# Kernel tuning notes

Hardware: AMD Instinct MI355X
Metric: run time of the kernel (lower is better)

## Reference

```python
import jax, jax.numpy as jnp
import numpy as np
import math

DIM = 1024
N_HEADS = 16
HEAD_DIM = DIM // N_HEADS
MAX_LEN = 4096
THETA = 10000.0
LN_EPS = 1e-5


def _rope_tables(dim, max_len, theta=THETA):
    # matches precompute_rope: freqs over even indices, angles = outer(t, freqs)
    inv = 1.0 / theta ** (np.arange(0, dim, 2, dtype=np.float32) / dim)
    t = np.arange(max_len, dtype=np.float32)
    ang = np.outer(t, inv)  # [max_len, dim//2]
    return jnp.asarray(np.cos(ang)), jnp.asarray(np.sin(ang))


def setup_inputs() -> dict:
    key = jax.random.key(0)
    ks = jax.random.split(key, 5)
    B, T, D = 2, 2048, DIM
    s = 1.0 / math.sqrt(D)
    x = jax.random.normal(ks[0], (B, T, D), dtype=jnp.float32)
    wq = jax.random.normal(ks[1], (D, D), dtype=jnp.float32) * s
    wk = jax.random.normal(ks[2], (D, D), dtype=jnp.float32) * s
    wv = jax.random.normal(ks[3], (D, D), dtype=jnp.float32) * s
    wo = jax.random.normal(ks[4], (D, D), dtype=jnp.float32) * s
    ln_g = jnp.ones((D,), dtype=jnp.float32)
    ln_b = jnp.zeros((D,), dtype=jnp.float32)
    cos, sin = _rope_tables(HEAD_DIM, MAX_LEN)
    return {"x": x, "wq": wq, "wk": wk, "wv": wv, "wo": wo,
            "ln_g": ln_g, "ln_b": ln_b, "cos": cos, "sin": sin}


def _rotate(x, cos, sin):
    # x: [B, T, H, hd]; complex multiply on interleaved (even, odd) pairs
    B, T, H, hd = x.shape
    xr = x.reshape(B, T, H, hd // 2, 2)
    x0, x1 = xr[..., 0], xr[..., 1]
    c = cos[None, :T, None, :]
    s = sin[None, :T, None, :]
    o0 = x0 * c - x1 * s
    o1 = x0 * s + x1 * c
    return jnp.stack([o0, o1], axis=-1).reshape(B, T, H, hd)


def reference(x, wq, wk, wv, wo, ln_g, ln_b, cos, sin):
    B, T, D = x.shape
    H, hd = N_HEADS, HEAD_DIM
    # LayerNorm
    mu = jnp.mean(x, axis=-1, keepdims=True)
    var = jnp.var(x, axis=-1, keepdims=True)
    h = (x - mu) * jax.lax.rsqrt(var + LN_EPS) * ln_g + ln_b
    # QKV projections (torch Linear: h @ W.T)
    q = jnp.einsum('btd,ed->bte', h, wq).reshape(B, T, H, hd)
    k = jnp.einsum('btd,ed->bte', h, wk).reshape(B, T, H, hd)
    v = jnp.einsum('btd,ed->bte', h, wv).reshape(B, T, H, hd)
    q = _rotate(q, cos, sin)
    k = _rotate(k, cos, sin)
    # full (non-causal) attention, scores [B, H, T, T]
    scores = jnp.einsum('bqhd,bkhd->bhqk', q, k) / math.sqrt(hd)
    attn = jax.nn.softmax(scores, axis=-1)
    out = jnp.einsum('bhqk,bkhd->bqhd', attn, v).reshape(B, T, D)
    return jnp.einsum('btd,ed->bte', out, wo)
```

## Files before the change

### kernel.cpp

```cpp
#include <hip/hip_runtime.h>
#include <hip/hip_bf16.h>

typedef __attribute__((ext_vector_type(4))) float          fx4;
typedef __attribute__((ext_vector_type(8))) __bf16         bfx8;
typedef __attribute__((ext_vector_type(8))) unsigned short usx8;
typedef __attribute__((ext_vector_type(4))) unsigned short usx4;

#define TLEN 2048
#define ROWS 4096
#define D    1024

__device__ __forceinline__ float bf2f(unsigned short u) {
    union { unsigned int i; float f; } v; v.i = ((unsigned int)u) << 16; return v.f;
}
__device__ __forceinline__ unsigned short f2bf(float f) {
    union { float f; unsigned int i; } v; v.f = f;
    unsigned int r = v.i + 0x7fffu + ((v.i >> 16) & 1u);
    return (unsigned short)(r >> 16);
}
__device__ __forceinline__ unsigned int cvtpk_bf16(float lo, float hi) {
    unsigned int r;
    asm("v_cvt_pk_bf16_f32 %0, %1, %2" : "=v"(r) : "v"(lo), "v"(hi));
    return r;
}
__device__ __forceinline__ float fast_cos(float a) {
    float r; asm("v_cos_f32 %0, %1" : "=v"(r) : "v"(a)); return r;
}
__device__ __forceinline__ float fast_sin(float a) {
    float r; asm("v_sin_f32 %0, %1" : "=v"(r) : "v"(a)); return r;
}
__device__ __forceinline__ void gload_lds16(const unsigned short* g, unsigned short* l) {
    __builtin_amdgcn_global_load_lds((const __attribute__((address_space(1))) void*)g,
                                     (__attribute__((address_space(3))) void*)l, 16, 0, 0);
}

__device__ __forceinline__ usx4 cvt4(fx4 a) {
    usx4 o;
    #pragma unroll
    for (int j = 0; j < 4; j++) o[j] = f2bf(a[j]);
    return o;
}
__global__ __launch_bounds__(256) void prep_kernel(const float* __restrict__ x,
                                                   const float* __restrict__ g,
                                                   const float* __restrict__ bta,
                                                   const float* __restrict__ wq, const float* __restrict__ wk,
                                                   const float* __restrict__ wv, const float* __restrict__ wo,
                                                   unsigned short* __restrict__ hout,
                                                   unsigned short* __restrict__ wqkv,
                                                   unsigned short* __restrict__ wob) {
    const int tid = threadIdx.x;
    if (blockIdx.x >= 4096) {
        const int i = (blockIdx.x - 4096) * 256 + tid;
        ((usx4*)wqkv)[i]          = cvt4(((const fx4*)wq)[i]);
        ((usx4*)wqkv)[262144 + i] = cvt4(((const fx4*)wk)[i]);
        ((usx4*)wqkv)[524288 + i] = cvt4(((const fx4*)wv)[i]);
        ((usx4*)wob)[i]           = cvt4(((const fx4*)wo)[i]);
        return;
    }
    const int row = blockIdx.x;
    fx4 v = ((const fx4*)(x + (size_t)row * D))[tid];
    float s  = v[0] + v[1] + v[2] + v[3];
    float s2 = v[0]*v[0] + v[1]*v[1] + v[2]*v[2] + v[3]*v[3];
    #pragma unroll
    for (int mk = 32; mk >= 1; mk >>= 1) { s += __shfl_xor(s, mk); s2 += __shfl_xor(s2, mk); }
    __shared__ float red[8];
    const int wave = tid >> 6, lane = tid & 63;
    if (lane == 0) { red[wave] = s; red[4 + wave] = s2; }
    __syncthreads();
    s  = red[0] + red[1] + red[2] + red[3];
    s2 = red[4] + red[5] + red[6] + red[7];
    float mu   = s * (1.0f / D);
    float var  = s2 * (1.0f / D) - mu * mu;
    float rstd = rsqrtf(var + 1e-5f);
    fx4 gv = ((const fx4*)g)[tid];
    fx4 bv = ((const fx4*)bta)[tid];
    usx4 o;
    #pragma unroll
    for (int j = 0; j < 4; j++) o[j] = f2bf((v[j] - mu) * rstd * gv[j] + bv[j]);
    ((usx4*)hout)[(size_t)row * 256 + tid] = o;
}

__global__ __launch_bounds__(256) void qkvt_gemm(const unsigned short* __restrict__ hbuf,
                                                 const unsigned short* __restrict__ wqkv,
                                                 unsigned short* __restrict__ qkout,
                                                 unsigned short* __restrict__ vtout) {
    constexpr int K = 1024;
    __shared__ __align__(16) unsigned short As[128 * 32];
    __shared__ __align__(16) unsigned short Bs[128 * 32];
    const int tid = threadIdx.x, lane = tid & 63, wave = tid >> 6;
    const int fr = lane & 15, fq = lane >> 4;
    const int wr = wave >> 1, wc = wave & 1;

    const int id = blockIdx.x;
    const bool isqk = id < 512;
    int bm, bn;
    const unsigned short *Ab, *Bb;
    if (isqk) {
        bm = id & 31; bn = id >> 5;
        Ab = hbuf + (size_t)(bm * 128) * K;
        Bb = wqkv + (size_t)(bn * 128) * K;
    } else {
        int j = id - 512; bm = j & 7; bn = j >> 3;
        Ab = wqkv + (size_t)(2048 * 1024) + (size_t)(bm * 128) * K;
        Bb = hbuf + (size_t)(bn * 128) * K;
    }

    const int str0 = wave * 32 + (lane >> 2);
    const int stc  = (lane & 3) * 8;

    fx4 acc[4][4];
    #pragma unroll
    for (int m = 0; m < 4; m++)
        #pragma unroll
        for (int n = 0; n < 4; n++) acc[m][n] = (fx4)0.0f;

    for (int kt = 0; kt < K; kt += 32) {
        gload_lds16(Ab + (size_t)str0 * K + kt + stc,        &As[str0 * 32 + stc]);
        gload_lds16(Ab + (size_t)(str0 + 16) * K + kt + stc, &As[(str0 + 16) * 32 + stc]);
        gload_lds16(Bb + (size_t)str0 * K + kt + stc,        &Bs[str0 * 32 + stc]);
        gload_lds16(Bb + (size_t)(str0 + 16) * K + kt + stc, &Bs[(str0 + 16) * 32 + stc]);
        __syncthreads();
        bfx8 aF[4], bF[4];
        #pragma unroll
        for (int m = 0; m < 4; m++) aF[m] = *(const bfx8*)&As[(wr * 64 + m * 16 + fr) * 32 + fq * 8];
        #pragma unroll
        for (int n = 0; n < 4; n++) bF[n] = *(const bfx8*)&Bs[(wc * 64 + n * 16 + fr) * 32 + fq * 8];
        #pragma unroll
        for (int m = 0; m < 4; m++)
            #pragma unroll
            for (int n = 0; n < 4; n++)
                acc[m][n] = __builtin_amdgcn_mfma_f32_16x16x32_bf16(aF[m], bF[n], acc[m][n], 0, 0, 0);
        __syncthreads();
    }

    const int row0 = bm * 128 + wr * 64 + fq * 4;
    const int col0 = bn * 128 + wc * 64 + fr;
    if (isqk) {
        const float QS = 0.125f * 1.44269504088896f;
        const bool isq = bn < 8;
        const float sgn = (fr & 1) ? 1.0f : -1.0f;
        float fp[4];
        #pragma unroll
        for (int n = 0; n < 4; n++) {
            float pif = (float)(n * 8 + (fr >> 1));
            fp[n] = __builtin_amdgcn_exp2f(fmaf(pif, -0.415241011861f, -2.651496129472f));
        }
        #pragma unroll
        for (int m = 0; m < 4; m++) {
            const int rbase = row0 + m * 16;
            const float tf = (float)(rbase & (TLEN - 1));
            #pragma unroll
            for (int n = 0; n < 4; n++) {
                #pragma unroll
                for (int j = 0; j < 4; j++) {
                    float a = __builtin_amdgcn_fractf((tf + (float)j) * fp[n]);
                    float c = fast_cos(a), s = fast_sin(a);
                    float self = acc[m][n][j];
                    float other = __shfl_xor(self, 1);
                    float o = self * c + other * (sgn * s);
                    if (isq) o *= QS;
                    qkout[(size_t)(rbase + j) * 2048 + col0 + n * 16] = f2bf(o);
                }
            }
        }
    } else {
        const int bb = bn >> 4;
        #pragma unroll
        for (int m = 0; m < 4; m++)
            #pragma unroll
            for (int n = 0; n < 4; n++) {
                const int t = (col0 + n * 16) & (TLEN - 1);
                const int tp = (t & ~63) | ((n >> 1) * 32 + ((fr >> 2)) * 8 + ((n & 1)) * 4 + (fr & 3));
                #pragma unroll
                for (int j = 0; j < 4; j++) {
                    const int d = row0 + m * 16 + j;
                    vtout[(((size_t)(bb * 16 + (d >> 6)) * 64) + (d & 63)) * TLEN + tp] = f2bf(acc[m][n][j]);
                }
            }
    }
}

__global__ __launch_bounds__(256) void gemm_out64(const unsigned short* __restrict__ A,
                                                  const unsigned short* __restrict__ B,
                                                  float* __restrict__ C) {
    constexpr int K = 1024;
    __shared__ __align__(16) unsigned short As[128 * 32];
    __shared__ __align__(16) unsigned short Bs[64 * 32];
    const int tid = threadIdx.x, lane = tid & 63, wave = tid >> 6;
    const int fr = lane & 15, fq = lane >> 4;
    const int bm = blockIdx.x, bn = blockIdx.y;
    const int wr = wave >> 1, wc = wave & 1;

    const int strA = wave * 32 + (lane >> 2);
    const int strB = wave * 16 + (lane >> 2);
    const int stc  = (lane & 3) * 8;
    const unsigned short* Ab = A + (size_t)(bm * 128) * K;
    const unsigned short* Bb = B + (size_t)(bn * 64) * K;

    fx4 acc[4][2];
    #pragma unroll
    for (int m = 0; m < 4; m++)
        #pragma unroll
        for (int n = 0; n < 2; n++) acc[m][n] = (fx4)0.0f;

    for (int kt = 0; kt < K; kt += 32) {
        gload_lds16(Ab + (size_t)strA * K + kt + stc,        &As[strA * 32 + stc]);
        gload_lds16(Ab + (size_t)(strA + 16) * K + kt + stc, &As[(strA + 16) * 32 + stc]);
        gload_lds16(Bb + (size_t)strB * K + kt + stc,        &Bs[strB * 32 + stc]);
        __syncthreads();
        bfx8 aF[4], bF[2];
        #pragma unroll
        for (int m = 0; m < 4; m++) aF[m] = *(const bfx8*)&As[(wr * 64 + m * 16 + fr) * 32 + fq * 8];
        #pragma unroll
        for (int n = 0; n < 2; n++) bF[n] = *(const bfx8*)&Bs[(wc * 32 + n * 16 + fr) * 32 + fq * 8];
        #pragma unroll
        for (int m = 0; m < 4; m++)
            #pragma unroll
            for (int n = 0; n < 2; n++)
                acc[m][n] = __builtin_amdgcn_mfma_f32_16x16x32_bf16(aF[m], bF[n], acc[m][n], 0, 0, 0);
        __syncthreads();
    }

    const int row0 = bm * 128 + wr * 64 + fq * 4;
    const int col0 = bn * 64 + wc * 32 + fr;
    #pragma unroll
    for (int m = 0; m < 4; m++)
        #pragma unroll
        for (int n = 0; n < 2; n++)
            #pragma unroll
            for (int j = 0; j < 4; j++)
                C[(size_t)(row0 + m * 16 + j) * 1024 + col0 + n * 16] = acc[m][n][j];
}

__global__ __launch_bounds__(256) void attn_kernel(const unsigned short* __restrict__ qk,
                                                   const unsigned short* __restrict__ vt,
                                                   unsigned short* __restrict__ ao) {
    const int flat = blockIdx.x + (blockIdx.y << 4);
    const int sid  = (flat & 7) * 64 + (flat >> 3);
    const int qt = sid & 15, bh = sid >> 4;
    const int b = bh >> 4, hh = bh & 15;
    const int tid = threadIdx.x, lane = tid & 63, wave = tid >> 6;
    const int fr = lane & 15, fq = lane >> 4;

    __shared__ __align__(16) unsigned short sK[2][64 * 64];
    __shared__ __align__(16) unsigned short sVt[2][64 * 64];

    const size_t rs = 2048;
    const unsigned short* qb  = qk + (size_t)b * TLEN * rs + hh * 64;
    const unsigned short* kb  = qb + 1024;
    const unsigned short* vtb = vt + (size_t)bh * (64 * TLEN);

    bfx8 qF[2][2];
    #pragma unroll
    for (int g = 0; g < 2; g++) {
        int qrow = qt * 128 + g * 64 + wave * 16 + fr;
        const unsigned short* qp = qb + (size_t)qrow * rs + fq * 8;
        qF[g][0] = *(const bfx8*)qp;
        qF[g][1] = *(const bfx8*)(qp + 32);
    }
    union { unsigned short us[8]; bfx8 bf; } ones_u;
    #pragma unroll
    for (int i = 0; i < 8; i++) ones_u.us[i] = 0x3F80;

    const int srow = lane >> 3;
    const int scol = ((lane & 7) ^ srow) * 8;

    #pragma unroll
    for (int i = 0; i < 2; i++) {
        int rg = wave * 2 + i;
        gload_lds16(kb  + (size_t)(rg * 8 + srow) * rs + scol,   &sK[0][rg * 512 + lane * 8]);
        gload_lds16(vtb + (size_t)(rg * 8 + srow) * TLEN + scol, &sVt[0][rg * 512 + lane * 8]);
    }

    float m_run[2] = {0.0f, 0.0f};
    fx4 oacc[2][4];
    fx4 oextra[2] = {(fx4)0.0f, (fx4)0.0f};
    #pragma unroll
    for (int g = 0; g < 2; g++)
        #pragma unroll
        for (int db = 0; db < 4; db++) oacc[g][db] = (fx4)0.0f;

    #pragma unroll 2
    for (int t = 0; t < 32; ++t) {
        const int buf = t & 1;
        __syncthreads();

        if (t + 1 < 32) {
            const int kt = (t + 1) * 64;
            #pragma unroll
            for (int i = 0; i < 2; i++) {
                int rg = wave * 2 + i;
                gload_lds16(kb  + (size_t)(kt + rg * 8 + srow) * rs + scol,
                            &sK[buf ^ 1][rg * 512 + lane * 8]);
                gload_lds16(vtb + (size_t)(rg * 8 + srow) * TLEN + kt + scol,
                            &sVt[buf ^ 1][rg * 512 + lane * 8]);
            }
        }

        bfx8 kF[2][4];
        #pragma unroll
        for (int s = 0; s < 2; s++)
            #pragma unroll
            for (int n = 0; n < 4; n++)
                kF[s][n] = *(const bfx8*)&sK[buf][(n * 16 + fr) * 64 + (((s * 4 + fq) ^ (fr & 7)) * 8)];
        fx4 sacc0[4], sacc1[4];
        #pragma unroll
        for (int n = 0; n < 4; n++) { sacc0[n] = (fx4)(-m_run[0]); sacc1[n] = (fx4)(-m_run[1]); }
        __builtin_amdgcn_s_setprio(1);
        #pragma unroll
        for (int s = 0; s < 2; s++)
            #pragma unroll
            for (int n = 0; n < 4; n++)
                sacc0[n] = __builtin_amdgcn_mfma_f32_16x16x32_bf16(kF[s][n], qF[0][s], sacc0[n], 0, 0, 0);
        #pragma unroll
        for (int s = 0; s < 2; s++)
            #pragma unroll
            for (int n = 0; n < 4; n++)
                sacc1[n] = __builtin_amdgcn_mfma_f32_16x16x32_bf16(kF[s][n], qF[1][s], sacc1[n], 0, 0, 0);
        __builtin_amdgcn_s_setprio(0);

        unsigned int u0[4][2];
        {
            float t0 = fmaxf(fmaxf(sacc0[0][0], sacc0[0][1]), sacc0[0][2]);
            float t1 = fmaxf(fmaxf(sacc0[0][3], sacc0[1][0]), sacc0[1][1]);
            float t2 = fmaxf(fmaxf(sacc0[1][2], sacc0[1][3]), sacc0[2][0]);
            float t3 = fmaxf(fmaxf(sacc0[2][1], sacc0[2][2]), sacc0[2][3]);
            float t4 = fmaxf(fmaxf(sacc0[3][0], sacc0[3][1]), sacc0[3][2]);
            float smax = fmaxf(fmaxf(fmaxf(t0, t1), t2), fmaxf(fmaxf(t3, t4), sacc0[3][3]));
            if (!__all(smax <= 8.0f)) {
                smax = fmaxf(smax, __shfl_xor(smax, 16));
                smax = fmaxf(smax, __shfl_xor(smax, 32));
                float delta = fmaxf(smax, 0.0f);
                float scal = __builtin_amdgcn_exp2f(-delta);
                m_run[0] += delta;
                #pragma unroll
                for (int n = 0; n < 4; n++)
                    #pragma unroll
                    for (int j = 0; j < 4; j++) sacc0[n][j] -= delta;
                #pragma unroll
                for (int db = 0; db < 4; db++) oacc[0][db] *= scal;
                oextra[0] *= scal;
            }
            #pragma unroll
            for (int n = 0; n < 4; n++) {
                float plo0 = __builtin_amdgcn_exp2f(sacc0[n][0]);
                float phi0 = __builtin_amdgcn_exp2f(sacc0[n][1]);
                float plo1 = __builtin_amdgcn_exp2f(sacc0[n][2]);
                float phi1 = __builtin_amdgcn_exp2f(sacc0[n][3]);
                u0[n][0] = cvtpk_bf16(plo0, phi0);
                u0[n][1] = cvtpk_bf16(plo1, phi1);
            }
        }

        bfx8 vF[2][4];
        #pragma unroll
        for (int s = 0; s < 2; s++)
            #pragma unroll
            for (int db = 0; db < 4; db++)
                vF[s][db] = *(const bfx8*)&sVt[buf][(db * 16 + fr) * 64 + (((s * 4 + fq) ^ (fr & 7)) * 8)];

        __builtin_amdgcn_s_setprio(1);
        #pragma unroll
        for (int s = 0; s < 2; s++) {
            union { unsigned int ui[4]; bfx8 bf; } cv;
            cv.ui[0] = u0[2 * s][0];     cv.ui[1] = u0[2 * s][1];
            cv.ui[2] = u0[2 * s + 1][0]; cv.ui[3] = u0[2 * s + 1][1];
            #pragma unroll
            for (int db = 0; db < 4; db++)
                oacc[0][db] = __builtin_amdgcn_mfma_f32_16x16x32_bf16(vF[s][db], cv.bf, oacc[0][db], 0, 0, 0);
            oextra[0] = __builtin_amdgcn_mfma_f32_16x16x32_bf16(ones_u.bf, cv.bf, oextra[0], 0, 0, 0);
        }
        __builtin_amdgcn_s_setprio(0);

        unsigned int u1[4][2];
        {
            float t0 = fmaxf(fmaxf(sacc1[0][0], sacc1[0][1]), sacc1[0][2]);
            float t1 = fmaxf(fmaxf(sacc1[0][3], sacc1[1][0]), sacc1[1][1]);
            float t2 = fmaxf(fmaxf(sacc1[1][2], sacc1[1][3]), sacc1[2][0]);
            float t3 = fmaxf(fmaxf(sacc1[2][1], sacc1[2][2]), sacc1[2][3]);
            float t4 = fmaxf(fmaxf(sacc1[3][0], sacc1[3][1]), sacc1[3][2]);
            float smax = fmaxf(fmaxf(fmaxf(t0, t1), t2), fmaxf(fmaxf(t3, t4), sacc1[3][3]));
            if (!__all(smax <= 8.0f)) {
                smax = fmaxf(smax, __shfl_xor(smax, 16));
                smax = fmaxf(smax, __shfl_xor(smax, 32));
                float delta = fmaxf(smax, 0.0f);
                float scal = __builtin_amdgcn_exp2f(-delta);
                m_run[1] += delta;
                #pragma unroll
                for (int n = 0; n < 4; n++)
                    #pragma unroll
                    for (int j = 0; j < 4; j++) sacc1[n][j] -= delta;
                #pragma unroll
                for (int db = 0; db < 4; db++) oacc[1][db] *= scal;
                oextra[1] *= scal;
            }
            #pragma unroll
            for (int n = 0; n < 4; n++) {
                float plo0 = __builtin_amdgcn_exp2f(sacc1[n][0]);
                float phi0 = __builtin_amdgcn_exp2f(sacc1[n][1]);
                float plo1 = __builtin_amdgcn_exp2f(sacc1[n][2]);
                float phi1 = __builtin_amdgcn_exp2f(sacc1[n][3]);
                u1[n][0] = cvtpk_bf16(plo0, phi0);
                u1[n][1] = cvtpk_bf16(plo1, phi1);
            }
        }

        __builtin_amdgcn_s_setprio(1);
        #pragma unroll
        for (int s = 0; s < 2; s++) {
            union { unsigned int ui[4]; bfx8 bf; } cv;
            cv.ui[0] = u1[2 * s][0];     cv.ui[1] = u1[2 * s][1];
            cv.ui[2] = u1[2 * s + 1][0]; cv.ui[3] = u1[2 * s + 1][1];
            #pragma unroll
            for (int db = 0; db < 4; db++)
                oacc[1][db] = __builtin_amdgcn_mfma_f32_16x16x32_bf16(vF[s][db], cv.bf, oacc[1][db], 0, 0, 0);
            oextra[1] = __builtin_amdgcn_mfma_f32_16x16x32_bf16(ones_u.bf, cv.bf, oextra[1], 0, 0, 0);
        }
        __builtin_amdgcn_s_setprio(0);
    }

    #pragma unroll
    for (int g = 0; g < 2; g++) {
        float invl = 1.0f / oextra[g][0];
        const int qrow = qt * 128 + g * 64 + wave * 16 + fr;
        unsigned short* aop = ao + (size_t)(b * TLEN + qrow) * 1024 + hh * 64 + fq * 4;
        #pragma unroll
        for (int db = 0; db < 4; db++) {
            usx4 o4;
            #pragma unroll
            for (int j = 0; j < 4; j++) o4[j] = f2bf(oacc[g][db][j] * invl);
            *(usx4*)(aop + db * 16) = o4;
        }
    }
}

extern "C" void kernel_launch(void* const* d_in, const int* in_sizes, int n_in,
                              void* d_out, int out_size, void* d_ws, size_t ws_size,
                              hipStream_t stream) {
    const float* x    = (const float*)d_in[0];
    const float* wq   = (const float*)d_in[1];
    const float* wk   = (const float*)d_in[2];
    const float* wv   = (const float*)d_in[3];
    const float* wo   = (const float*)d_in[4];
    const float* lng  = (const float*)d_in[5];
    const float* lnb  = (const float*)d_in[6];

    char* ws = (char*)d_ws;
    unsigned short* wob  = (unsigned short*)(ws);
    unsigned short* wqkv = (unsigned short*)(ws + (2u  << 20));
    unsigned short* hbuf = (unsigned short*)(ws + (8u  << 20));
    unsigned short* qk   = (unsigned short*)(ws + (16u << 20));
    unsigned short* vtb  = (unsigned short*)(ws + (32u << 20));
    unsigned short* ao   = (unsigned short*)(ws + (8u  << 20));

    prep_kernel<<<5120, 256, 0, stream>>>(x, lng, lnb, wq, wk, wv, wo, hbuf, wqkv, wob);
    qkvt_gemm<<<768, 256, 0, stream>>>(hbuf, wqkv, qk, vtb);
    attn_kernel<<<dim3(16, 32), 256, 0, stream>>>(qk, vtb, ao);
    gemm_out64<<<dim3(32, 16), 256, 0, stream>>>(ao, wob, (float*)d_out);
}
```

Baseline: 127.4 us.

## Double-buffer GEMM LDS tiles and widen attention KV tiles to 128 keys

Both GEMM kernels now double-buffer their LDS tiles. The next K-slice is prefetched while MFMAs run on the current one, and one barrier per iteration is dropped. The attention kernel processes 128 keys per iteration instead of 64. This halves loop trips and barriers and interleaves the two query groups' MFMAs to share K/V fragment loads. The V-transpose layout written by the QKV GEMM changes to match the new 128-wide swizzle. The cost is higher LDS use and register pressure, which may lower occupancy.

```diff
diff --git a/kernel.cpp b/kernel.cpp
--- a/kernel.cpp
+++ b/kernel.cpp
@@ -85,8 +85,8 @@
                                                  unsigned short* __restrict__ qkout,
                                                  unsigned short* __restrict__ vtout) {
     constexpr int K = 1024;
-    __shared__ __align__(16) unsigned short As[128 * 32];
-    __shared__ __align__(16) unsigned short Bs[128 * 32];
+    __shared__ __align__(16) unsigned short As[2][128 * 32];
+    __shared__ __align__(16) unsigned short Bs[2][128 * 32];
     const int tid = threadIdx.x, lane = tid & 63, wave = tid >> 6;
     const int fr = lane & 15, fq = lane >> 4;
     const int wr = wave >> 1, wc = wave & 1;
@@ -114,23 +114,31 @@
         #pragma unroll
         for (int n = 0; n < 4; n++) acc[m][n] = (fx4)0.0f;
 
+    gload_lds16(Ab + (size_t)str0 * K + stc,        &As[0][str0 * 32 + stc]);
+    gload_lds16(Ab + (size_t)(str0 + 16) * K + stc, &As[0][(str0 + 16) * 32 + stc]);
+    gload_lds16(Bb + (size_t)str0 * K + stc,        &Bs[0][str0 * 32 + stc]);
+    gload_lds16(Bb + (size_t)(str0 + 16) * K + stc, &Bs[0][(str0 + 16) * 32 + stc]);
+
+    #pragma unroll 2
     for (int kt = 0; kt < K; kt += 32) {
-        gload_lds16(Ab + (size_t)str0 * K + kt + stc,        &As[str0 * 32 + stc]);
-        gload_lds16(Ab + (size_t)(str0 + 16) * K + kt + stc, &As[(str0 + 16) * 32 + stc]);
-        gload_lds16(Bb + (size_t)str0 * K + kt + stc,        &Bs[str0 * 32 + stc]);
-        gload_lds16(Bb + (size_t)(str0 + 16) * K + kt + stc, &Bs[(str0 + 16) * 32 + stc]);
+        const int b = (kt >> 5) & 1;
         __syncthreads();
+        if (kt + 32 < K) {
+            gload_lds16(Ab + (size_t)str0 * K + kt + 32 + stc,        &As[b ^ 1][str0 * 32 + stc]);
+            gload_lds16(Ab + (size_t)(str0 + 16) * K + kt + 32 + stc, &As[b ^ 1][(str0 + 16) * 32 + stc]);
+            gload_lds16(Bb + (size_t)str0 * K + kt + 32 + stc,        &Bs[b ^ 1][str0 * 32 + stc]);
+            gload_lds16(Bb + (size_t)(str0 + 16) * K + kt + 32 + stc, &Bs[b ^ 1][(str0 + 16) * 32 + stc]);
+        }
         bfx8 aF[4], bF[4];
         #pragma unroll
-        for (int m = 0; m < 4; m++) aF[m] = *(const bfx8*)&As[(wr * 64 + m * 16 + fr) * 32 + fq * 8];
-        #pragma unroll
-        for (int n = 0; n < 4; n++) bF[n] = *(const bfx8*)&Bs[(wc * 64 + n * 16 + fr) * 32 + fq * 8];
+        for (int m = 0; m < 4; m++) aF[m] = *(const bfx8*)&As[b][(wr * 64 + m * 16 + fr) * 32 + fq * 8];
+        #pragma unroll
+        for (int n = 0; n < 4; n++) bF[n] = *(const bfx8*)&Bs[b][(wc * 64 + n * 16 + fr) * 32 + fq * 8];
         #pragma unroll
         for (int m = 0; m < 4; m++)
             #pragma unroll
             for (int n = 0; n < 4; n++)
                 acc[m][n] = __builtin_amdgcn_mfma_f32_16x16x32_bf16(aF[m], bF[n], acc[m][n], 0, 0, 0);
-        __syncthreads();
     }
 
     const int row0 = bm * 128 + wr * 64 + fq * 4;
@@ -169,8 +177,9 @@
         for (int m = 0; m < 4; m++)
             #pragma unroll
             for (int n = 0; n < 4; n++) {
+                const int np = wc * 4 + n;
                 const int t = (col0 + n * 16) & (TLEN - 1);
-                const int tp = (t & ~63) | ((n >> 1) * 32 + ((fr >> 2)) * 8 + ((n & 1)) * 4 + (fr & 3));
+                const int tp = (t & ~127) | ((np >> 1) * 32 + ((fr >> 2)) * 8 + ((np & 1)) * 4 + (fr & 3));
                 #pragma unroll
                 for (int j = 0; j < 4; j++) {
                     const int d = row0 + m * 16 + j;
@@ -184,8 +193,8 @@
                                                   const unsigned short* __restrict__ B,
                                                   float* __restrict__ C) {
     constexpr int K = 1024;
-    __shared__ __align__(16) unsigned short As[128 * 32];
-    __shared__ __align__(16) unsigned short Bs[64 * 32];
+    __shared__ __align__(16) unsigned short As[2][128 * 32];
+    __shared__ __align__(16) unsigned short Bs[2][64 * 32];
     const int tid = threadIdx.x, lane = tid & 63, wave = tid >> 6;
     const int fr = lane & 15, fq = lane >> 4;
     const int bm = blockIdx.x, bn = blockIdx.y;
@@ -203,22 +212,29 @@
         #pragma unroll
         for (int n = 0; n < 2; n++) acc[m][n] = (fx4)0.0f;
 
+    gload_lds16(Ab + (size_t)strA * K + stc,        &As[0][strA * 32 + stc]);
+    gload_lds16(Ab + (size_t)(strA + 16) * K + stc, &As[0][(strA + 16) * 32 + stc]);
+    gload_lds16(Bb + (size_t)strB * K + stc,        &Bs[0][strB * 32 + stc]);
+
+    #pragma unroll 2
     for (int kt = 0; kt < K; kt += 32) {
-        gload_lds16(Ab + (size_t)strA * K + kt + stc,        &As[strA * 32 + stc]);
-        gload_lds16(Ab + (size_t)(strA + 16) * K + kt + stc, &As[(strA + 16) * 32 + stc]);
-        gload_lds16(Bb + (size_t)strB * K + kt + stc,        &Bs[strB * 32 + stc]);
+        const int b = (kt >> 5) & 1;
         __syncthreads();
+        if (kt + 32 < K) {
+            gload_lds16(Ab + (size_t)strA * K + kt + 32 + stc,        &As[b ^ 1][strA * 32 + stc]);
+            gload_lds16(Ab + (size_t)(strA + 16) * K + kt + 32 + stc, &As[b ^ 1][(strA + 16) * 32 + stc]);
+            gload_lds16(Bb + (size_t)strB * K + kt + 32 + stc,        &Bs[b ^ 1][strB * 32 + stc]);
+        }
         bfx8 aF[4], bF[2];
         #pragma unroll
-        for (int m = 0; m < 4; m++) aF[m] = *(const bfx8*)&As[(wr * 64 + m * 16 + fr) * 32 + fq * 8];
-        #pragma unroll
-        for (int n = 0; n < 2; n++) bF[n] = *(const bfx8*)&Bs[(wc * 32 + n * 16 + fr) * 32 + fq * 8];
+        for (int m = 0; m < 4; m++) aF[m] = *(const bfx8*)&As[b][(wr * 64 + m * 16 + fr) * 32 + fq * 8];
+        #pragma unroll
+        for (int n = 0; n < 2; n++) bF[n] = *(const bfx8*)&Bs[b][(wc * 32 + n * 16 + fr) * 32 + fq * 8];
         #pragma unroll
         for (int m = 0; m < 4; m++)
             #pragma unroll
             for (int n = 0; n < 2; n++)
                 acc[m][n] = __builtin_amdgcn_mfma_f32_16x16x32_bf16(aF[m], bF[n], acc[m][n], 0, 0, 0);
-        __syncthreads();
     }
 
     const int row0 = bm * 128 + wr * 64 + fq * 4;
@@ -242,8 +258,8 @@
     const int tid = threadIdx.x, lane = tid & 63, wave = tid >> 6;
     const int fr = lane & 15, fq = lane >> 4;
 
-    __shared__ __align__(16) unsigned short sK[2][64 * 64];
-    __shared__ __align__(16) unsigned short sVt[2][64 * 64];
+    __shared__ __align__(16) unsigned short sK[2][128 * 64];
+    __shared__ __align__(16) unsigned short sVt[2][64 * 128];
 
     const size_t rs = 2048;
     const unsigned short* qb  = qk + (size_t)b * TLEN * rs + hh * 64;
@@ -263,14 +279,25 @@
     for (int i = 0; i < 8; i++) ones_u.us[i] = 0x3F80;
 
     const int srow = lane >> 3;
-    const int scol = ((lane & 7) ^ srow) * 8;
-
-    #pragma unroll
-    for (int i = 0; i < 2; i++) {
-        int rg = wave * 2 + i;
-        gload_lds16(kb  + (size_t)(rg * 8 + srow) * rs + scol,   &sK[0][rg * 512 + lane * 8]);
-        gload_lds16(vtb + (size_t)(rg * 8 + srow) * TLEN + scol, &sVt[0][rg * 512 + lane * 8]);
-    }
+    const int scolK = ((lane & 7) ^ srow) * 8;
+    const int vr = lane >> 4;
+    const int vc = lane & 15;
+
+    #define STAGE_ATTN(BUF, KT)                                                        \
+        {                                                                              \
+            _Pragma("unroll")                                                          \
+            for (int i = 0; i < 4; i++) {                                              \
+                int rg = wave * 4 + i;                                                 \
+                gload_lds16(kb + (size_t)((KT) + rg * 8 + srow) * rs + scolK,          \
+                            &sK[BUF][rg * 512 + lane * 8]);                            \
+                int g2 = wave * 4 + i;                                                 \
+                int key = ((i & 1) << 2) | vr;                                         \
+                gload_lds16(vtb + (size_t)(g2 * 4 + vr) * TLEN + (KT) + ((vc ^ key) * 8), \
+                            &sVt[BUF][g2 * 512 + lane * 8]);                           \
+            }                                                                          \
+        }
+
+    STAGE_ATTN(0, 0)
 
     float m_run[2] = {0.0f, 0.0f};
     fx4 oacc[2][4];
@@ -281,52 +308,34 @@
         for (int db = 0; db < 4; db++) oacc[g][db] = (fx4)0.0f;
 
     #pragma unroll 2
-    for (int t = 0; t < 32; ++t) {
+    for (int t = 0; t < 16; ++t) {
         const int buf = t & 1;
         __syncthreads();
 
-        if (t + 1 < 32) {
-            const int kt = (t + 1) * 64;
-            #pragma unroll
-            for (int i = 0; i < 2; i++) {
-                int rg = wave * 2 + i;
-                gload_lds16(kb  + (size_t)(kt + rg * 8 + srow) * rs + scol,
-                            &sK[buf ^ 1][rg * 512 + lane * 8]);
-                gload_lds16(vtb + (size_t)(rg * 8 + srow) * TLEN + kt + scol,
-                            &sVt[buf ^ 1][rg * 512 + lane * 8]);
-            }
-        }
-
-        bfx8 kF[2][4];
+        if (t + 1 < 16) STAGE_ATTN(buf ^ 1, (t + 1) * 128)
+
+        fx4 s0[8], s1[8];
+        #pragma unroll
+        for (int n = 0; n < 8; n++) { s0[n] = (fx4)(-m_run[0]); s1[n] = (fx4)(-m_run[1]); }
+        __builtin_amdgcn_s_setprio(1);
         #pragma unroll
         for (int s = 0; s < 2; s++)
             #pragma unroll
-            for (int n = 0; n < 4; n++)
-                kF[s][n] = *(const bfx8*)&sK[buf][(n * 16 + fr) * 64 + (((s * 4 + fq) ^ (fr & 7)) * 8)];
-        fx4 sacc0[4], sacc1[4];
-        #pragma unroll
-        for (int n = 0; n < 4; n++) { sacc0[n] = (fx4)(-m_run[0]); sacc1[n] = (fx4)(-m_run[1]); }
-        __builtin_amdgcn_s_setprio(1);
-        #pragma unroll
-        for (int s = 0; s < 2; s++)
-            #pragma unroll
-            for (int n = 0; n < 4; n++)
-                sacc0[n] = __builtin_amdgcn_mfma_f32_16x16x32_bf16(kF[s][n], qF[0][s], sacc0[n], 0, 0, 0);
-        #pragma unroll
-        for (int s = 0; s < 2; s++)
-            #pragma unroll
-            for (int n = 0; n < 4; n++)
-                sacc1[n] = __builtin_amdgcn_mfma_f32_16x16x32_bf16(kF[s][n], qF[1][s], sacc1[n], 0, 0, 0);
+            for (int n = 0; n < 8; n++) {
+                bfx8 kF = *(const bfx8*)&sK[buf][(n * 16 + fr) * 64 + (((s * 4 + fq) ^ (fr & 7)) * 8)];
+                s0[n] = __builtin_amdgcn_mfma_f32_16x16x32_bf16(kF, qF[0][s], s0[n], 0, 0, 0);
+                s1[n] = __builtin_amdgcn_mfma_f32_16x16x32_bf16(kF, qF[1][s], s1[n], 0, 0, 0);
+            }
         __builtin_amdgcn_s_setprio(0);
 
-        unsigned int u0[4][2];
+        unsigned int u0[8][2], u1[8][2];
         {
-            float t0 = fmaxf(fmaxf(sacc0[0][0], sacc0[0][1]), sacc0[0][2]);
-            float t1 = fmaxf(fmaxf(sacc0[0][3], sacc0[1][0]), sacc0[1][1]);
-            float t2 = fmaxf(fmaxf(sacc0[1][2], sacc0[1][3]), sacc0[2][0]);
-            float t3 = fmaxf(fmaxf(sacc0[2][1], sacc0[2][2]), sacc0[2][3]);
-            float t4 = fmaxf(fmaxf(sacc0[3][0], sacc0[3][1]), sacc0[3][2]);
-            float smax = fmaxf(fmaxf(fmaxf(t0, t1), t2), fmaxf(fmaxf(t3, t4), sacc0[3][3]));
+            float pm[8];
+            #pragma unroll
+            for (int n = 0; n < 8; n++)
+                pm[n] = fmaxf(fmaxf(s0[n][0], s0[n][1]), fmaxf(s0[n][2], s0[n][3]));
+            float smax = fmaxf(fmaxf(fmaxf(pm[0], pm[1]), fmaxf(pm[2], pm[3])),
+                               fmaxf(fmaxf(pm[4], pm[5]), fmaxf(pm[6], pm[7])));
             if (!__all(smax <= 8.0f)) {
                 smax = fmaxf(smax, __shfl_xor(smax, 16));
                 smax = fmaxf(smax, __shfl_xor(smax, 32));
@@ -334,52 +343,26 @@
                 float scal = __builtin_amdgcn_exp2f(-delta);
                 m_run[0] += delta;
                 #pragma unroll
-                for (int n = 0; n < 4; n++)
+                for (int n = 0; n < 8; n++)
                     #pragma unroll
-                    for (int j = 0; j < 4; j++) sacc0[n][j] -= delta;
+                    for (int j = 0; j < 4; j++) s0[n][j] -= delta;
                 #pragma unroll
                 for (int db = 0; db < 4; db++) oacc[0][db] *= scal;
                 oextra[0] *= scal;
             }
             #pragma unroll
-            for (int n = 0; n < 4; n++) {
-                float plo0 = __builtin_amdgcn_exp2f(sacc0[n][0]);
-                float phi0 = __builtin_amdgcn_exp2f(sacc0[n][1]);
-                float plo1 = __builtin_amdgcn_exp2f(sacc0[n][2]);
-                float phi1 = __builtin_amdgcn_exp2f(sacc0[n][3]);
-                u0[n][0] = cvtpk_bf16(plo0, phi0);
-                u0[n][1] = cvtpk_bf16(plo1, phi1);
-            }
-        }
-
-        bfx8 vF[2][4];
-        #pragma unroll
-        for (int s = 0; s < 2; s++)
-            #pragma unroll
-            for (int db = 0; db < 4; db++)
-                vF[s][db] = *(const bfx8*)&sVt[buf][(db * 16 + fr) * 64 + (((s * 4 + fq) ^ (fr & 7)) * 8)];
-
-        __builtin_amdgcn_s_setprio(1);
-        #pragma unroll
-        for (int s = 0; s < 2; s++) {
-            union { unsigned int ui[4]; bfx8 bf; } cv;
-            cv.ui[0] = u0[2 * s][0];     cv.ui[1] = u0[2 * s][1];
-            cv.ui[2] = u0[2 * s + 1][0]; cv.ui[3] = u0[2 * s + 1][1];
-            #pragma unroll
-            for (int db = 0; db < 4; db++)
-                oacc[0][db] = __builtin_amdgcn_mfma_f32_16x16x32_bf16(vF[s][db], cv.bf, oacc[0][db], 0, 0, 0);
-            oextra[0] = __builtin_amdgcn_mfma_f32_16x16x32_bf16(ones_u.bf, cv.bf, oextra[0], 0, 0, 0);
-        }
-        __builtin_amdgcn_s_setprio(0);
-
-        unsigned int u1[4][2];
+            for (int n = 0; n < 8; n++) {
+                u0[n][0] = cvtpk_bf16(__builtin_amdgcn_exp2f(s0[n][0]), __builtin_amdgcn_exp2f(s0[n][1]));
+                u0[n][1] = cvtpk_bf16(__builtin_amdgcn_exp2f(s0[n][2]), __builtin_amdgcn_exp2f(s0[n][3]));
+            }
+        }
         {
-            float t0 = fmaxf(fmaxf(sacc1[0][0], sacc1[0][1]), sacc1[0][2]);
-            float t1 = fmaxf(fmaxf(sacc1[0][3], sacc1[1][0]), sacc1[1][1]);
-            float t2 = fmaxf(fmaxf(sacc1[1][2], sacc1[1][3]), sacc1[2][0]);
-            float t3 = fmaxf(fmaxf(sacc1[2][1], sacc1[2][2]), sacc1[2][3]);
-            float t4 = fmaxf(fmaxf(sacc1[3][0], sacc1[3][1]), sacc1[3][2]);
-            float smax = fmaxf(fmaxf(fmaxf(t0, t1), t2), fmaxf(fmaxf(t3, t4), sacc1[3][3]));
+            float pm[8];
+            #pragma unroll
+            for (int n = 0; n < 8; n++)
+                pm[n] = fmaxf(fmaxf(s1[n][0], s1[n][1]), fmaxf(s1[n][2], s1[n][3]));
+            float smax = fmaxf(fmaxf(fmaxf(pm[0], pm[1]), fmaxf(pm[2], pm[3])),
+                               fmaxf(fmaxf(pm[4], pm[5]), fmaxf(pm[6], pm[7])));
             if (!__all(smax <= 8.0f)) {
                 smax = fmaxf(smax, __shfl_xor(smax, 16));
                 smax = fmaxf(smax, __shfl_xor(smax, 32));
@@ -387,37 +370,40 @@
                 float scal = __builtin_amdgcn_exp2f(-delta);
                 m_run[1] += delta;
                 #pragma unroll
-                for (int n = 0; n < 4; n++)
+                for (int n = 0; n < 8; n++)
                     #pragma unroll
-                    for (int j = 0; j < 4; j++) sacc1[n][j] -= delta;
+                    for (int j = 0; j < 4; j++) s1[n][j] -= delta;
                 #pragma unroll
                 for (int db = 0; db < 4; db++) oacc[1][db] *= scal;
                 oextra[1] *= scal;
             }
             #pragma unroll
-            for (int n = 0; n < 4; n++) {
-                float plo0 = __builtin_amdgcn_exp2f(sacc1[n][0]);
-                float phi0 = __builtin_amdgcn_exp2f(sacc1[n][1]);
-                float plo1 = __builtin_amdgcn_exp2f(sacc1[n][2]);
-                float phi1 = __builtin_amdgcn_exp2f(sacc1[n][3]);
-                u1[n][0] = cvtpk_bf16(plo0, phi0);
-                u1[n][1] = cvtpk_bf16(plo1, phi1);
+            for (int n = 0; n < 8; n++) {
+                u1[n][0] = cvtpk_bf16(__builtin_amdgcn_exp2f(s1[n][0]), __builtin_amdgcn_exp2f(s1[n][1]));
+                u1[n][1] = cvtpk_bf16(__builtin_amdgcn_exp2f(s1[n][2]), __builtin_amdgcn_exp2f(s1[n][3]));
             }
         }
 
         __builtin_amdgcn_s_setprio(1);
         #pragma unroll
-        for (int s = 0; s < 2; s++) {
-            union { unsigned int ui[4]; bfx8 bf; } cv;
-            cv.ui[0] = u1[2 * s][0];     cv.ui[1] = u1[2 * s][1];
-            cv.ui[2] = u1[2 * s + 1][0]; cv.ui[3] = u1[2 * s + 1][1];
-            #pragma unroll
-            for (int db = 0; db < 4; db++)
-                oacc[1][db] = __builtin_amdgcn_mfma_f32_16x16x32_bf16(vF[s][db], cv.bf, oacc[1][db], 0, 0, 0);
-            oextra[1] = __builtin_amdgcn_mfma_f32_16x16x32_bf16(ones_u.bf, cv.bf, oextra[1], 0, 0, 0);
+        for (int sp = 0; sp < 4; sp++) {
+            union { unsigned int ui[4]; bfx8 bf; } c0, c1;
+            c0.ui[0] = u0[2 * sp][0];     c0.ui[1] = u0[2 * sp][1];
+            c0.ui[2] = u0[2 * sp + 1][0]; c0.ui[3] = u0[2 * sp + 1][1];
+            c1.ui[0] = u1[2 * sp][0];     c1.ui[1] = u1[2 * sp][1];
+            c1.ui[2] = u1[2 * sp + 1][0]; c1.ui[3] = u1[2 * sp + 1][1];
+            #pragma unroll
+            for (int db = 0; db < 4; db++) {
+                bfx8 vF = *(const bfx8*)&sVt[buf][(db * 16 + fr) * 128 + (((sp * 4 + fq) ^ (fr & 7)) * 8)];
+                oacc[0][db] = __builtin_amdgcn_mfma_f32_16x16x32_bf16(vF, c0.bf, oacc[0][db], 0, 0, 0);
+                oacc[1][db] = __builtin_amdgcn_mfma_f32_16x16x32_bf16(vF, c1.bf, oacc[1][db], 0, 0, 0);
+            }
+            oextra[0] = __builtin_amdgcn_mfma_f32_16x16x32_bf16(ones_u.bf, c0.bf, oextra[0], 0, 0, 0);
+            oextra[1] = __builtin_amdgcn_mfma_f32_16x16x32_bf16(ones_u.bf, c1.bf, oextra[1], 0, 0, 0);
         }
         __builtin_amdgcn_s_setprio(0);
     }
+    #undef STAGE_ATTN
 
     #pragma unroll
     for (int g = 0; g < 2; g++) {
```

Result: slower. 151.8 us (+19.2%).

## Halve attention block to 2 waves and 64 query rows, doubling grid

Applied to the files above, without the earlier changes.

The attention kernel now uses 128 threads (2 waves) per block covering 64 query rows instead of 256 threads covering 128 rows. The grid doubles to 1024 blocks, and each wave stages twice as many K/V rows into LDS per tile. The aim is more blocks to spread across CUs and a smaller tail. In exchange, K/V tiles are reused by half as many queries, so global/LDS traffic per unit of work roughly doubles. The exp/convert code is only reformatted.

```diff
diff --git a/kernel.cpp b/kernel.cpp
--- a/kernel.cpp
+++ b/kernel.cpp
@@ -232,12 +232,12 @@
                 C[(size_t)(row0 + m * 16 + j) * 1024 + col0 + n * 16] = acc[m][n][j];
 }
 
-__global__ __launch_bounds__(256) void attn_kernel(const unsigned short* __restrict__ qk,
+__global__ __launch_bounds__(128) void attn_kernel(const unsigned short* __restrict__ qk,
                                                    const unsigned short* __restrict__ vt,
                                                    unsigned short* __restrict__ ao) {
-    const int flat = blockIdx.x + (blockIdx.y << 4);
-    const int sid  = (flat & 7) * 64 + (flat >> 3);
-    const int qt = sid & 15, bh = sid >> 4;
+    const int flat = blockIdx.x + (blockIdx.y << 5);
+    const int sid  = (flat & 7) * 128 + (flat >> 3);
+    const int qt = sid & 31, bh = sid >> 5;
     const int b = bh >> 4, hh = bh & 15;
     const int tid = threadIdx.x, lane = tid & 63, wave = tid >> 6;
     const int fr = lane & 15, fq = lane >> 4;
@@ -253,7 +253,7 @@
     bfx8 qF[2][2];
     #pragma unroll
     for (int g = 0; g < 2; g++) {
-        int qrow = qt * 128 + g * 64 + wave * 16 + fr;
+        int qrow = qt * 64 + g * 32 + wave * 16 + fr;
         const unsigned short* qp = qb + (size_t)qrow * rs + fq * 8;
         qF[g][0] = *(const bfx8*)qp;
         qF[g][1] = *(const bfx8*)(qp + 32);
@@ -265,12 +265,19 @@
     const int srow = lane >> 3;
     const int scol = ((lane & 7) ^ srow) * 8;
 
-    #pragma unroll
-    for (int i = 0; i < 2; i++) {
-        int rg = wave * 2 + i;
-        gload_lds16(kb  + (size_t)(rg * 8 + srow) * rs + scol,   &sK[0][rg * 512 + lane * 8]);
-        gload_lds16(vtb + (size_t)(rg * 8 + srow) * TLEN + scol, &sVt[0][rg * 512 + lane * 8]);
-    }
+    #define STAGE_ATTN(BUF, KT)                                                      \
+        {                                                                            \
+            _Pragma("unroll")                                                        \
+            for (int i = 0; i < 4; i++) {                                            \
+                int rg = wave * 4 + i;                                               \
+                gload_lds16(kb  + (size_t)((KT) + rg * 8 + srow) * rs + scol,        \
+                            &sK[BUF][rg * 512 + lane * 8]);                          \
+                gload_lds16(vtb + (size_t)(rg * 8 + srow) * TLEN + (KT) + scol,      \
+                            &sVt[BUF][rg * 512 + lane * 8]);                         \
+            }                                                                        \
+        }
+
+    STAGE_ATTN(0, 0)
 
     float m_run[2] = {0.0f, 0.0f};
     fx4 oacc[2][4];
@@ -285,17 +292,7 @@
         const int buf = t & 1;
         __syncthreads();
 
-        if (t + 1 < 32) {
-            const int kt = (t + 1) * 64;
-            #pragma unroll
-            for (int i = 0; i < 2; i++) {
-                int rg = wave * 2 + i;
-                gload_lds16(kb  + (size_t)(kt + rg * 8 + srow) * rs + scol,
-                            &sK[buf ^ 1][rg * 512 + lane * 8]);
-                gload_lds16(vtb + (size_t)(rg * 8 + srow) * TLEN + kt + scol,
-                            &sVt[buf ^ 1][rg * 512 + lane * 8]);
-            }
-        }
+        if (t + 1 < 32) STAGE_ATTN(buf ^ 1, (t + 1) * 64)
 
         bfx8 kF[2][4];
         #pragma unroll
@@ -319,7 +316,7 @@
                 sacc1[n] = __builtin_amdgcn_mfma_f32_16x16x32_bf16(kF[s][n], qF[1][s], sacc1[n], 0, 0, 0);
         __builtin_amdgcn_s_setprio(0);
 
-        unsigned int u0[4][2];
+        unsigned int u0[4][2], u1[4][2];
         {
             float t0 = fmaxf(fmaxf(sacc0[0][0], sacc0[0][1]), sacc0[0][2]);
             float t1 = fmaxf(fmaxf(sacc0[0][3], sacc0[1][0]), sacc0[1][1]);
@@ -343,12 +340,8 @@
             }
             #pragma unroll
             for (int n = 0; n < 4; n++) {
-                float plo0 = __builtin_amdgcn_exp2f(sacc0[n][0]);
-                float phi0 = __builtin_amdgcn_exp2f(sacc0[n][1]);
-                float plo1 = __builtin_amdgcn_exp2f(sacc0[n][2]);
-                float phi1 = __builtin_amdgcn_exp2f(sacc0[n][3]);
-                u0[n][0] = cvtpk_bf16(plo0, phi0);
-                u0[n][1] = cvtpk_bf16(plo1, phi1);
+                u0[n][0] = cvtpk_bf16(__builtin_amdgcn_exp2f(sacc0[n][0]), __builtin_amdgcn_exp2f(sacc0[n][1]));
+                u0[n][1] = cvtpk_bf16(__builtin_amdgcn_exp2f(sacc0[n][2]), __builtin_amdgcn_exp2f(sacc0[n][3]));
             }
         }
 
@@ -372,7 +365,6 @@
         }
         __builtin_amdgcn_s_setprio(0);
 
-        unsigned int u1[4][2];
         {
             float t0 = fmaxf(fmaxf(sacc1[0][0], sacc1[0][1]), sacc1[0][2]);
             float t1 = fmaxf(fmaxf(sacc1[0][3], sacc1[1][0]), sacc1[1][1]);
@@ -396,12 +388,8 @@
             }
             #pragma unroll
             for (int n = 0; n < 4; n++) {
-                float plo0 = __builtin_amdgcn_exp2f(sacc1[n][0]);
-                float phi0 = __builtin_amdgcn_exp2f(sacc1[n][1]);
-                float plo1 = __builtin_amdgcn_exp2f(sacc1[n][2]);
-                float phi1 = __builtin_amdgcn_exp2f(sacc1[n][3]);
-                u1[n][0] = cvtpk_bf16(plo0, phi0);
-                u1[n][1] = cvtpk_bf16(plo1, phi1);
+                u1[n][0] = cvtpk_bf16(__builtin_amdgcn_exp2f(sacc1[n][0]), __builtin_amdgcn_exp2f(sacc1[n][1]));
+                u1[n][1] = cvtpk_bf16(__builtin_amdgcn_exp2f(sacc1[n][2]), __builtin_amdgcn_exp2f(sacc1[n][3]));
             }
         }
 
@@ -418,11 +406,12 @@
         }
         __builtin_amdgcn_s_setprio(0);
     }
+    #undef STAGE_ATTN
 
     #pragma unroll
     for (int g = 0; g < 2; g++) {
         float invl = 1.0f / oextra[g][0];
-        const int qrow = qt * 128 + g * 64 + wave * 16 + fr;
+        const int qrow = qt * 64 + g * 32 + wave * 16 + fr;
         unsigned short* aop = ao + (size_t)(b * TLEN + qrow) * 1024 + hh * 64 + fq * 4;
         #pragma unroll
         for (int db = 0; db < 4; db++) {
@@ -455,6 +444,6 @@
 
     prep_kernel<<<5120, 256, 0, stream>>>(x, lng, lnb, wq, wk, wv, wo, hbuf, wqkv, wob);
     qkvt_gemm<<<768, 256, 0, stream>>>(hbuf, wqkv, qk, vtb);
-    attn_kernel<<<dim3(16, 32), 256, 0, stream>>>(qk, vtb, ao);
+    attn_kernel<<<dim3(32, 32), 128, 0, stream>>>(qk, vtb, ao);
     gemm_out64<<<dim3(32, 16), 256, 0, stream>>>(ao, wob, (float*)d_out);
 }
```

Result: slower. 130.5 us (+2.4%).
